# Kernel tuning notes

Measured on AMD Instinct MI355X. Metric: run time of the kernel, lower is better.

The kernel has to match this reference:

```python
import jax, jax.numpy as jnp
import numpy as np

B, S, E = 2, 2048, 4096
HQ, HKV, D = 32, 8, 128
WINDOW = 1024
SOFT_CAP = 50.0
Q_PRE_ATTN = 128.0
TT_SCALE = 0.1
TT_FLOOR = 8192.0
EPS = 1e-6
ROPE_BASE = 10000.0


def l2norm(x):
    return x * jax.lax.rsqrt(jnp.mean(x * x, axis=-1, keepdims=True) + EPS)


def apply_rope(x, pos):
    # x: [B,S,H,D]; half-split rotary, base 10000
    half = x.shape[-1] // 2
    freq = ROPE_BASE ** (-jnp.arange(half, dtype=jnp.float32) * 2.0 / x.shape[-1])  # [half]
    angle = pos.astype(jnp.float32)[:, None] * freq[None, :]                         # [S,half]
    cos = jnp.cos(angle)[None, :, None, :]
    sin = jnp.sin(angle)[None, :, None, :]
    x1, x2 = x[..., :half], x[..., half:]
    return jnp.concatenate([x1 * cos - x2 * sin, x2 * cos + x1 * sin], axis=-1)


def setup_inputs() -> dict:
    key = jax.random.key(0)
    ks = jax.random.split(key, 5)
    sc = 0.02
    return {
        "x": jax.random.normal(ks[0], (B, S, E), jnp.float32),
        "Wq": jax.random.normal(ks[1], (E, HQ, D), jnp.float32) * sc,
        "Wk": jax.random.normal(ks[2], (E, HKV, D), jnp.float32) * sc,
        "Wv": jax.random.normal(ks[3], (E, HKV, D), jnp.float32) * sc,
        "Wo": jax.random.normal(ks[4], (HQ, D, E), jnp.float32) * sc,
    }


def reference(x, Wq, Wk, Wv, Wo):
    pos = jnp.arange(S)
    # QKV projections
    q = jnp.einsum('bse,ehd->bshd', x, Wq)   # [B,S,HQ,D]
    k = jnp.einsum('bse,ehd->bshd', x, Wk)   # [B,S,HKV,D]
    v = jnp.einsum('bse,ehd->bshd', x, Wv)   # [B,S,HKV,D]
    # QK norm (L2Norm) then RoPE
    q = apply_rope(l2norm(q), pos)
    k = apply_rope(l2norm(k), pos)
    # query pre-attention scaling
    q = q * (Q_PRE_ATTN ** -0.5)
    # temperature tuning: per-position scale
    attn_scale = jnp.log(jnp.floor((pos.astype(jnp.float32) + 1.0) / TT_FLOOR) + 1.0) * TT_SCALE + 1.0
    q = q * attn_scale[None, :, None, None]
    # GQA: expand kv heads
    g = HQ // HKV
    k_r = jnp.repeat(k, g, axis=2)           # [B,S,HQ,D]
    v_r = jnp.repeat(v, g, axis=2)
    logits = jnp.einsum('bihd,bjhd->bhij', q, k_r).astype(jnp.float32)
    # tanh soft cap
    logits = SOFT_CAP * jnp.tanh(logits / SOFT_CAP)
    # causal + sliding window mask: j <= i and i - j < WINDOW
    i = pos[:, None]
    j = pos[None, :]
    mask = (j <= i) & ((i - j) < WINDOW)     # [S,S]
    logits = jnp.where(mask[None, None], logits, jnp.float32(-1e30))
    probs = jax.nn.softmax(logits, axis=-1)
    out = jnp.einsum('bhij,bjhd->bihd', probs, v_r)  # [B,S,HQ,D]
    return jnp.einsum('bihd,hde->bie', out, Wo)      # [B,S,E]
```

## Files before the change

kernel.cpp:

```cpp
#include <hip/hip_runtime.h>


typedef unsigned short u16;
typedef unsigned int   u32;
typedef __bf16 bf16x8 __attribute__((ext_vector_type(8)));
typedef float  f32x4  __attribute__((ext_vector_type(4)));

typedef __attribute__((address_space(1))) void* gas_ptr;
typedef __attribute__((address_space(3))) void* las_ptr;

__device__ __forceinline__ void load_lds16(const void* g, void* l) {
  __builtin_amdgcn_global_load_lds((gas_ptr)g, (las_ptr)l, 16, 0, 0);
}

__device__ __forceinline__ u16 f2bf(float f) {
  u32 u = __builtin_bit_cast(u32, f);
  u += 0x7fffu + ((u >> 16) & 1u);
  return (u16)(u >> 16);
}
__device__ __forceinline__ float bf2f(u16 h) {
  u32 u = ((u32)h) << 16;
  return __builtin_bit_cast(float, u);
}
__device__ __forceinline__ u32 pack_trunc(float a, float b) {
  return (__builtin_bit_cast(u32, a) >> 16) | (__builtin_bit_cast(u32, b) & 0xffff0000u);
}

__global__ __launch_bounds__(256) void cast_f32_bf16(const float* __restrict__ src,
                                                     u16* __restrict__ dst) {
  size_t i = ((size_t)blockIdx.x * 256 + threadIdx.x) * 8;
  float4 a = *(const float4*)(src + i);
  float4 b = *(const float4*)(src + i + 4);
  uint4 o;
  o.x = (u32)f2bf(a.x) | ((u32)f2bf(a.y) << 16);
  o.y = (u32)f2bf(a.z) | ((u32)f2bf(a.w) << 16);
  o.z = (u32)f2bf(b.x) | ((u32)f2bf(b.y) << 16);
  o.w = (u32)f2bf(b.z) | ((u32)f2bf(b.w) << 16);
  *(uint4*)(dst + i) = o;
}

__global__ __launch_bounds__(256) void transpose_cast_f32_bf16(
    const float* __restrict__ src, u16* __restrict__ dst, int R, int C) {
  __shared__ float tile[32][33];
  const int tx = threadIdx.x & 31, ty = threadIdx.x >> 5;
  const int r0 = blockIdx.y * 32, c0 = blockIdx.x * 32;
#pragma unroll
  for (int i = 0; i < 4; ++i)
    tile[ty + i * 8][tx] = src[(size_t)(r0 + ty + i * 8) * C + (c0 + tx)];
  __syncthreads();
#pragma unroll
  for (int i = 0; i < 4; ++i)
    dst[(size_t)(c0 + ty + i * 8) * R + (r0 + tx)] = f2bf(tile[tx][ty + i * 8]);
}

__global__ __launch_bounds__(256) void transpose_v(const u16* __restrict__ src,
                                                   u16* __restrict__ dst) {
  __shared__ u16 tile[32][34];
  const int plane = blockIdx.z;
  const u16* s = src + (size_t)plane * 2048 * 128;
  u16* d = dst + (size_t)plane * 2048 * 128;
  const int tx = threadIdx.x & 31, ty = threadIdx.x >> 5;
  const int r0 = blockIdx.x * 32, c0 = blockIdx.y * 32;
#pragma unroll
  for (int i = 0; i < 4; ++i)
    tile[ty + i * 8][tx] = s[(size_t)(r0 + ty + i * 8) * 128 + (c0 + tx)];
  __syncthreads();
#pragma unroll
  for (int i = 0; i < 4; ++i)
    d[(size_t)(c0 + ty + i * 8) * 2048 + (r0 + tx)] = tile[tx][ty + i * 8];
}


template <int MB>
__device__ __forceinline__ void mm16(f32x4 (&acc)[8][4], const bf16x8 (&af)[4],
                                     const bf16x8 (&bf)[4]) {
#pragma unroll
  for (int ii = 0; ii < 4; ++ii)
#pragma unroll
    for (int nf = 0; nf < 4; ++nf)
      acc[MB + ii][nf] =
          __builtin_amdgcn_mfma_f32_16x16x32_bf16(af[ii], bf[nf], acc[MB + ii][nf], 0, 0, 0);
}

template <int OUT_BF16>
__global__ __launch_bounds__(512, 2) void gemm256(const u16* __restrict__ A,
                                                  const u16* __restrict__ Bt,
                                                  void* __restrict__ Cout,
                                                  int N, int K, int ntx) {
  __shared__ __align__(16) u16 lds[65536];
  const int t = threadIdx.x, lane = t & 63, w = t >> 6;
  const int c = lane & 15, q = lane >> 4;
  const int wm = w >> 2, wn = w & 3;

  const int cpx = (int)gridDim.x >> 3;
  const int swz = ((int)blockIdx.x & 7) * cpx + ((int)blockIdx.x >> 3);
  const int bx = swz % ntx, by = swz / ntx;
  const int m0 = by << 8, n0 = bx << 8;

  u32 aoff[2][2], boff[2][2];
#pragma unroll
  for (int h = 0; h < 2; ++h)
#pragma unroll
    for (int j = 0; j < 2; ++j) {
      const int rowS = w * 16 + j * 8 + (lane >> 3);
      const int colE = ((lane & 7) ^ (rowS & 7)) * 8;
      aoff[h][j] = (u32)(m0 + h * 128 + rowS) * (u32)K + (u32)colE;
      boff[h][j] = (u32)(n0 + h * 128 + rowS) * (u32)K + (u32)colE;
    }
  const u32 stW = (u32)w * 1024u;

  const u32 sl0 = (u32)((q ^ (c & 7)) * 8);
  const u32 aR = (u32)(wm * 8192 + c * 64) + sl0;
  const u32 bR = (u32)(16384 + (wn >> 1) * 8192 + (wn & 1) * 4096 + c * 64) + sl0;

  f32x4 acc[8][4];
#pragma unroll
  for (int i2 = 0; i2 < 8; ++i2)
#pragma unroll
    for (int j2 = 0; j2 < 4; ++j2) acc[i2][j2] = (f32x4){0.f, 0.f, 0.f, 0.f};

  const int nt = K >> 6;

#define STG_A(bb, hh, kt)                                                \
  do {                                                                   \
    u16* d_ = &lds[(bb) * 32768u + (hh) * 8192u + stW];                  \
    load_lds16(A + (aoff[hh][0] + (u32)(kt) * 64u), d_);                 \
    load_lds16(A + (aoff[hh][1] + (u32)(kt) * 64u), d_ + 512);           \
  } while (0)
#define STG_B(bb, hh, kt)                                                \
  do {                                                                   \
    u16* d_ = &lds[(bb) * 32768u + 16384u + (hh) * 8192u + stW];         \
    load_lds16(Bt + (boff[hh][0] + (u32)(kt) * 64u), d_);                \
    load_lds16(Bt + (boff[hh][1] + (u32)(kt) * 64u), d_ + 512);          \
  } while (0)
#define RD4(dst, base)                                                   \
  do {                                                                   \
    const u16* p_ = &lds[(base)];                                        \
    dst[0] = *(const bf16x8*)(p_);                                       \
    dst[1] = *(const bf16x8*)(p_ + 1024);                                \
    dst[2] = *(const bf16x8*)(p_ + 2048);                                \
    dst[3] = *(const bf16x8*)(p_ + 3072);                                \
  } while (0)
#define BAR __builtin_amdgcn_s_barrier()
#define LGKM0 asm volatile("s_waitcnt lgkmcnt(0)" ::: "memory")
#define VM6 asm volatile("s_waitcnt vmcnt(6)" ::: "memory")
#define PRIO1 __builtin_amdgcn_s_setprio(1)
#define PRIO0 __builtin_amdgcn_s_setprio(0)

  STG_B(0, 0, 0);
  STG_B(0, 1, 0);
  STG_A(0, 0, 0);
  STG_A(0, 1, 0);
  STG_B(1, 0, 1);
  STG_B(1, 1, 1);
  STG_A(1, 0, 1);
  VM6;
  BAR;

  bf16x8 Bf0[4], Bf1[4], Af0[4], Af1[4];

  for (int i = 0; i < (nt >> 1); ++i) {
    const int tb = 2 * i + 1;
    int t2 = 2 * i + 2; if (t2 >= nt) t2 -= nt;
    int t3 = 2 * i + 3; if (t3 >= nt) t3 -= nt;

    RD4(Bf0, bR);
    RD4(Bf1, bR ^ 32u);
    RD4(Af0, aR);
    STG_A(1, 1, tb);
    BAR; LGKM0;
    PRIO1; mm16<0>(acc, Af0, Bf0); PRIO0;
    BAR;
    RD4(Af1, aR + 4096u);
    STG_B(0, 0, t2);
    BAR; LGKM0;
    PRIO1; mm16<4>(acc, Af1, Bf0); PRIO0;
    BAR;
    RD4(Af0, aR ^ 32u);
    RD4(Af1, (aR + 4096u) ^ 32u);
    STG_B(0, 1, t2);
    BAR; LGKM0;
    PRIO1; mm16<0>(acc, Af0, Bf1); PRIO0;
    BAR;
    STG_A(0, 0, t2);
    VM6;
    BAR;
    PRIO1; mm16<4>(acc, Af1, Bf1); PRIO0;
    BAR;

    RD4(Bf0, 32768u + bR);
    RD4(Bf1, (32768u + bR) ^ 32u);
    RD4(Af0, 32768u + aR);
    STG_A(0, 1, t2);
    BAR; LGKM0;
    PRIO1; mm16<0>(acc, Af0, Bf0); PRIO0;
    BAR;
    RD4(Af1, 32768u + aR + 4096u);
    STG_B(1, 0, t3);
    BAR; LGKM0;
    PRIO1; mm16<4>(acc, Af1, Bf0); PRIO0;
    BAR;
    RD4(Af0, (32768u + aR) ^ 32u);
    RD4(Af1, (32768u + aR + 4096u) ^ 32u);
    STG_B(1, 1, t3);
    BAR; LGKM0;
    PRIO1; mm16<0>(acc, Af0, Bf1); PRIO0;
    BAR;
    STG_A(1, 0, t3);
    VM6;
    BAR;
    PRIO1; mm16<4>(acc, Af1, Bf1); PRIO0;
    BAR;
  }

  asm volatile("s_waitcnt vmcnt(0)" ::: "memory");

#undef STG_A
#undef STG_B
#undef RD4
#undef BAR
#undef LGKM0
#undef VM6
#undef PRIO1
#undef PRIO0

  const int rb0 = m0 + wm * 128 + q * 4;
  const int cb0 = n0 + wn * 64 + c;
#pragma unroll
  for (int mf = 0; mf < 8; ++mf)
#pragma unroll
    for (int nf = 0; nf < 4; ++nf) {
      const size_t base = (size_t)(rb0 + mf * 16) * N + (cb0 + nf * 16);
#pragma unroll
      for (int r = 0; r < 4; ++r) {
        if (OUT_BF16)
          ((u16*)Cout)[base + (size_t)r * N] = f2bf(acc[mf][nf][r]);
        else
          ((float*)Cout)[base + (size_t)r * N] = acc[mf][nf][r];
      }
    }
}

__global__ __launch_bounds__(256) void qkv_post(const u16* __restrict__ raw,
                                                u16* __restrict__ qb,
                                                u16* __restrict__ kb,
                                                u16* __restrict__ vb) {
  const int t = threadIdx.x, lane = t & 63, w = t >> 6;
  const int idx = blockIdx.x * 4 + w;
  const int row = idx / 48, hh = idx - row * 48;
  const int b = row >> 11, pos = row & 2047;
  const u16* base = raw + (size_t)row * 6144 + hh * 128;
  const u16 r1 = base[lane], r2 = base[lane + 64];

  if (hh >= 40) {
    u16* dst = vb + ((size_t)((b * 8 + (hh - 40)) * 2048 + pos)) * 128;
    dst[lane] = r1;
    dst[lane + 64] = r2;
    return;
  }
  float v1 = bf2f(r1), v2 = bf2f(r2);
  float ss = v1 * v1 + v2 * v2;
#pragma unroll
  for (int off = 32; off >= 1; off >>= 1) ss += __shfl_xor(ss, off);
  const float rn = rsqrtf(ss * (1.0f / 128.0f) + 1e-6f);
  const float n1 = v1 * rn, n2 = v2 * rn;
  const float fr = exp2f(-(float)lane * 0.20762050593046f);
  const float ang = (float)pos * fr;
  float sn, cs;
  sincosf(ang, &sn, &cs);
  float o1 = n1 * cs - n2 * sn;
  float o2 = n2 * cs + n1 * sn;
  u16* dst;
  if (hh < 32) {
    const float as_ = logf(floorf((float)(pos + 1) * (1.0f / 8192.0f)) + 1.0f) * 0.1f + 1.0f;
    const float sc = 0.088388347648318447f * as_;
    o1 *= sc;
    o2 *= sc;
    dst = qb + ((size_t)((b * 32 + hh) * 2048 + pos)) * 128;
  } else {
    dst = kb + ((size_t)((b * 8 + (hh - 32)) * 2048 + pos)) * 128;
  }
  dst[lane] = f2bf(o1);
  dst[lane + 64] = f2bf(o2);
}

__global__ __launch_bounds__(256, 4) void attn_fwd(const u16* __restrict__ qb,
                                                   const u16* __restrict__ kb,
                                                   const u16* __restrict__ vtb,
                                                   u16* __restrict__ attn) {
  __shared__ __align__(16) u16 Ks[64 * 128];
  __shared__ __align__(16) u16 VTs[128 * 64];
  __shared__ __align__(16) u16 Ps[4][16 * 64];

  const int t = threadIdx.x, lane = t & 63, w = t >> 6;
  const int c = lane & 15, quad = lane >> 4;
  const int q0 = blockIdx.x * 64;
  const int bh = blockIdx.y;
  const int b = bh >> 5, hq = bh & 31;
  const int kvp = b * 8 + (hq >> 2);
  const u16* qp = qb + (size_t)bh * (2048 * 128);
  const u16* kp = kb + (size_t)kvp * (2048 * 128);
  const u16* vp = vtb + (size_t)kvp * (128 * 2048);
  u16* Psw = &Ps[w][0];

  bf16x8 qf[4];
  {
    const u16* qrow = qp + (size_t)(q0 + w * 16 + c) * 128 + quad * 8;
#pragma unroll
    for (int ks = 0; ks < 4; ++ks) qf[ks] = *(const bf16x8*)(qrow + ks * 32);
  }

  f32x4 oacc[8];
#pragma unroll
  for (int j = 0; j < 8; ++j)
#pragma unroll
    for (int r = 0; r < 4; ++r) oacc[j][r] = 0.0f;
  float lsum = 0.0f;

  const int i_glob = q0 + w * 16 + c;

  int t0 = q0 - 1023;
  if (t0 < 0) t0 = 0;
  t0 = (t0 >> 6) << 6;

  for (int kv0 = t0; kv0 <= q0; kv0 += 64) {
    __syncthreads();
    {
      const int row_in = lane >> 4, ch = lane & 15;
#pragma unroll
      for (int i = 0; i < 4; ++i) {
        const int row = w * 4 + i * 16 + row_in;
        const int g = ch ^ (row & 15);
        load_lds16(kp + (size_t)(kv0 + row) * 128 + g * 8, &Ks[(w * 4 + i * 16) * 128]);
      }
      const int drow = lane >> 3, ch8 = lane & 7;
#pragma unroll
      for (int i = 0; i < 4; ++i) {
        const int dd = w * 8 + i * 32 + drow;
        const int g = ch8 ^ (dd & 7);
        load_lds16(vp + (size_t)dd * 2048 + kv0 + g * 8, &VTs[(w * 8 + i * 32) * 64]);
      }
    }
    __syncthreads();

    f32x4 sacc[4];
#pragma unroll
    for (int im = 0; im < 4; ++im)
#pragma unroll
      for (int r = 0; r < 4; ++r) sacc[im][r] = 0.0f;

#pragma unroll
    for (int ks = 0; ks < 4; ++ks) {
#pragma unroll
      for (int im = 0; im < 4; ++im) {
        const int key = im * 16 + c;
        const int ch = (ks * 4 + quad) ^ c;
        const bf16x8 af = *(const bf16x8*)&Ks[key * 128 + ch * 8];
        sacc[im] = __builtin_amdgcn_mfma_f32_16x16x32_bf16(af, qf[ks], sacc[im], 0, 0, 0);
      }
    }

    const bool need_mask = (kv0 == q0) || (q0 - kv0 >= 961);
#pragma unroll
    for (int im = 0; im < 4; ++im) {
      float pv[4];
#pragma unroll
      for (int r = 0; r < 4; ++r) {
        const float s = sacc[im][r];
        const float u = s * s;
        const float cap = s * (1.0f + u * (-1.3333333e-4f + u * 2.1333333e-8f));
        pv[r] = __expf(cap);
      }
      if (need_mask) {
        const int j_base = kv0 + im * 16 + quad * 4;
#pragma unroll
        for (int r = 0; r < 4; ++r) {
          const int j_glob = j_base + r;
          if (!((j_glob <= i_glob) && (i_glob - j_glob < 1024))) pv[r] = 0.0f;
        }
      }
      lsum += (pv[0] + pv[1]) + (pv[2] + pv[3]);
      uint2 pk;
      pk.x = pack_trunc(pv[0], pv[1]);
      pk.y = pack_trunc(pv[2], pv[3]);
      *(uint2*)&Psw[c * 64 + ((im * 2 + (quad >> 1)) ^ (c & 7)) * 8 + (quad & 1) * 4] = pk;
    }

#pragma unroll
    for (int ks = 0; ks < 2; ++ks) {
      const bf16x8 pf = *(const bf16x8*)&Psw[c * 64 + ((ks * 4 + quad) ^ (c & 7)) * 8];
#pragma unroll
      for (int jn = 0; jn < 8; ++jn) {
        const int dd = jn * 16 + c;
        const int ch = (ks * 4 + quad) ^ (c & 7);
        const bf16x8 vf = *(const bf16x8*)&VTs[dd * 64 + ch * 8];
        oacc[jn] = __builtin_amdgcn_mfma_f32_16x16x32_bf16(pf, vf, oacc[jn], 0, 0, 0);
      }
    }
  }

  float lt = lsum;
  lt += __shfl_xor(lt, 16);
  lt += __shfl_xor(lt, 32);
  float rl[4];
#pragma unroll
  for (int r = 0; r < 4; ++r)
    rl[r] = __builtin_amdgcn_rcpf(__shfl(lt, quad * 4 + r));

  const size_t obase = ((size_t)(b * 2048 + q0 + w * 16)) * 4096 + hq * 128;
#pragma unroll
  for (int jn = 0; jn < 8; ++jn) {
#pragma unroll
    for (int r = 0; r < 4; ++r) {
      const int q_in = quad * 4 + r;
      attn[obase + (size_t)q_in * 4096 + jn * 16 + c] = f2bf(oacc[jn][r] * rl[r]);
    }
  }
}

extern "C" void kernel_launch(void* const* d_in, const int* in_sizes, int n_in,
                              void* d_out, int out_size, void* d_ws, size_t ws_size,
                              hipStream_t stream) {
  (void)in_sizes; (void)n_in; (void)out_size; (void)ws_size;
  const float* x  = (const float*)d_in[0];
  const float* Wq = (const float*)d_in[1];
  const float* Wk = (const float*)d_in[2];
  const float* Wv = (const float*)d_in[3];
  const float* Wo = (const float*)d_in[4];
  float* out = (float*)d_out;
  char* ws = (char*)d_ws;

  u16* xb    = (u16*)(ws + 0);
  u16* vtb   = (u16*)(ws + 0);
  u16* WqkvT = (u16*)(ws + 33554432ULL);
  u16* qb    = (u16*)(ws + 33554432ULL);
  u16* kb    = (u16*)(ws + 67108864ULL);
  u16* vb    = (u16*)(ws + 75497472ULL);
  u16* WoT   = (u16*)(ws + 83886080ULL);
  u16* qkvr  = (u16*)(ws + 117440512ULL);
  u16* attnb = (u16*)(ws + 117440512ULL);

  cast_f32_bf16<<<8192, 256, 0, stream>>>(x, xb);
  transpose_cast_f32_bf16<<<dim3(128, 128), 256, 0, stream>>>(Wq, WqkvT, 4096, 4096);
  transpose_cast_f32_bf16<<<dim3(32, 128), 256, 0, stream>>>(Wk, WqkvT + (size_t)4096 * 4096, 4096, 1024);
  transpose_cast_f32_bf16<<<dim3(32, 128), 256, 0, stream>>>(Wv, WqkvT + (size_t)5120 * 4096, 4096, 1024);
  transpose_cast_f32_bf16<<<dim3(128, 128), 256, 0, stream>>>(Wo, WoT, 4096, 4096);

  gemm256<1><<<dim3(384), 512, 0, stream>>>(xb, WqkvT, (void*)qkvr, 6144, 4096, 24);
  qkv_post<<<49152, 256, 0, stream>>>(qkvr, qb, kb, vb);
  transpose_v<<<dim3(64, 4, 16), 256, 0, stream>>>(vb, vtb);
  attn_fwd<<<dim3(32, 64), 256, 0, stream>>>(qb, kb, vtb, attnb);
  gemm256<0><<<dim3(256), 512, 0, stream>>>(attnb, WoT, (void*)out, 4096, 4096, 16);
}
```

Measured before the change: 710.1 us.

## Double-buffer K/V tiles in attention and add partial LDS waits in GEMM

The attention kernel now keeps two LDS buffers for K and V^T and issues the global-to-LDS load of the next KV tile before computing on the current one, with one barrier per iteration in place of two. The aim is to overlap global memory latency with the QK^T and PV MFMA work. The GEMM main loop also gains an lgkmcnt(8) wait before the barrier at two points to partly drain LDS reads earlier. The doubled LDS footprint (about 80KB per block) may cut occupancy below the launch_bounds target of 4 blocks per CU. It also depends on the vmcnt accounting of the barrier-ordered async loads being correct.

```diff
diff --git a/kernel.cpp b/kernel.cpp
--- a/kernel.cpp
+++ b/kernel.cpp
@@ -143,6 +143,7 @@
   } while (0)
 #define BAR __builtin_amdgcn_s_barrier()
 #define LGKM0 asm volatile("s_waitcnt lgkmcnt(0)" ::: "memory")
+#define LGKM8 asm volatile("s_waitcnt lgkmcnt(8)" ::: "memory")
 #define VM6 asm volatile("s_waitcnt vmcnt(6)" ::: "memory")
 #define PRIO1 __builtin_amdgcn_s_setprio(1)
 #define PRIO0 __builtin_amdgcn_s_setprio(0)
@@ -168,6 +169,7 @@
     RD4(Bf1, bR ^ 32u);
     RD4(Af0, aR);
     STG_A(1, 1, tb);
+    LGKM8;
     BAR; LGKM0;
     PRIO1; mm16<0>(acc, Af0, Bf0); PRIO0;
     BAR;
@@ -192,6 +194,7 @@
     RD4(Bf1, (32768u + bR) ^ 32u);
     RD4(Af0, 32768u + aR);
     STG_A(0, 1, t2);
+    LGKM8;
     BAR; LGKM0;
     PRIO1; mm16<0>(acc, Af0, Bf0); PRIO0;
     BAR;
@@ -220,6 +223,7 @@
 #undef RD4
 #undef BAR
 #undef LGKM0
+#undef LGKM8
 #undef VM6
 #undef PRIO1
 #undef PRIO0
@@ -288,8 +292,8 @@
                                                    const u16* __restrict__ kb,
                                                    const u16* __restrict__ vtb,
                                                    u16* __restrict__ attn) {
-  __shared__ __align__(16) u16 Ks[64 * 128];
-  __shared__ __align__(16) u16 VTs[128 * 64];
+  __shared__ __align__(16) u16 Ks[2][64 * 128];
+  __shared__ __align__(16) u16 VTs[2][128 * 64];
   __shared__ __align__(16) u16 Ps[4][16 * 64];
 
   const int t = threadIdx.x, lane = t & 63, w = t >> 6;
@@ -323,25 +327,35 @@
   if (t0 < 0) t0 = 0;
   t0 = (t0 >> 6) << 6;
 
+#define STAGE_KV(nb, kvbase)                                                   \
+  do {                                                                         \
+    const int row_in_ = lane >> 4, ch_ = lane & 15;                            \
+    _Pragma("unroll")                                                          \
+    for (int i_ = 0; i_ < 4; ++i_) {                                           \
+      const int row_ = w * 4 + i_ * 16 + row_in_;                              \
+      const int g_ = ch_ ^ (row_ & 15);                                        \
+      load_lds16(kp + (size_t)((kvbase) + row_) * 128 + g_ * 8,                \
+                 &Ks[nb][(w * 4 + i_ * 16) * 128]);                            \
+    }                                                                          \
+    const int drow_ = lane >> 3, ch8_ = lane & 7;                              \
+    _Pragma("unroll")                                                          \
+    for (int i_ = 0; i_ < 4; ++i_) {                                           \
+      const int dd_ = w * 8 + i_ * 32 + drow_;                                 \
+      const int g_ = ch8_ ^ (dd_ & 7);                                         \
+      load_lds16(vp + (size_t)dd_ * 2048 + (kvbase) + g_ * 8,                  \
+                 &VTs[nb][(w * 8 + i_ * 32) * 64]);                            \
+    }                                                                          \
+  } while (0)
+
+  STAGE_KV(0, t0);
+  __syncthreads();
+
+  int cur = 0;
   for (int kv0 = t0; kv0 <= q0; kv0 += 64) {
-    __syncthreads();
-    {
-      const int row_in = lane >> 4, ch = lane & 15;
-#pragma unroll
-      for (int i = 0; i < 4; ++i) {
-        const int row = w * 4 + i * 16 + row_in;
-        const int g = ch ^ (row & 15);
-        load_lds16(kp + (size_t)(kv0 + row) * 128 + g * 8, &Ks[(w * 4 + i * 16) * 128]);
-      }
-      const int drow = lane >> 3, ch8 = lane & 7;
-#pragma unroll
-      for (int i = 0; i < 4; ++i) {
-        const int dd = w * 8 + i * 32 + drow;
-        const int g = ch8 ^ (dd & 7);
-        load_lds16(vp + (size_t)dd * 2048 + kv0 + g * 8, &VTs[(w * 8 + i * 32) * 64]);
-      }
-    }
-    __syncthreads();
+    if (kv0 + 64 <= q0) STAGE_KV(cur ^ 1, kv0 + 64);
+
+    const u16* Kc = &Ks[cur][0];
+    const u16* Vc = &VTs[cur][0];
 
     f32x4 sacc[4];
 #pragma unroll
@@ -355,7 +369,7 @@
       for (int im = 0; im < 4; ++im) {
         const int key = im * 16 + c;
         const int ch = (ks * 4 + quad) ^ c;
-        const bf16x8 af = *(const bf16x8*)&Ks[key * 128 + ch * 8];
+        const bf16x8 af = *(const bf16x8*)&Kc[key * 128 + ch * 8];
         sacc[im] = __builtin_amdgcn_mfma_f32_16x16x32_bf16(af, qf[ks], sacc[im], 0, 0, 0);
       }
     }
@@ -393,11 +407,15 @@
       for (int jn = 0; jn < 8; ++jn) {
         const int dd = jn * 16 + c;
         const int ch = (ks * 4 + quad) ^ (c & 7);
-        const bf16x8 vf = *(const bf16x8*)&VTs[dd * 64 + ch * 8];
+        const bf16x8 vf = *(const bf16x8*)&Vc[dd * 64 + ch * 8];
         oacc[jn] = __builtin_amdgcn_mfma_f32_16x16x32_bf16(pf, vf, oacc[jn], 0, 0, 0);
       }
     }
-  }
+
+    __syncthreads();
+    cur ^= 1;
+  }
+#undef STAGE_KV
 
   float lt = lsum;
   lt += __shfl_xor(lt, 16);
```

Measured after the change: 725.2 us. 1.02x slower.
